# Kernel optimization log

Measured on AMD Instinct MI355X. Metric: run time of the kernel, lower is better.

The kernel has to match this reference:

```python
import jax, jax.numpy as jnp
import numpy as np

N_NODES = 100000
N_EDGES = 1600000
IN_FEATS = 256
H_FEATS = 256
NUM_CLASSES = 64


def setup_inputs() -> dict:
    key = jax.random.key(0)
    ks = jax.random.split(key, 7)
    x = jax.random.normal(ks[0], (N_NODES, IN_FEATS), dtype=jnp.float32)
    src = jax.random.randint(ks[1], (N_EDGES,), 0, N_NODES, dtype=jnp.int64)
    dst = jax.random.randint(ks[2], (N_EDGES,), 0, N_NODES, dtype=jnp.int64)
    W = jax.random.normal(ks[3], (IN_FEATS, H_FEATS), dtype=jnp.float32) / np.sqrt(IN_FEATS)
    b = jax.random.normal(ks[4], (H_FEATS,), dtype=jnp.float32) * 0.01
    W2 = jax.random.normal(ks[5], (H_FEATS, NUM_CLASSES), dtype=jnp.float32) / np.sqrt(H_FEATS)
    b2 = jax.random.normal(ks[6], (NUM_CLASSES,), dtype=jnp.float32) * 0.01
    return {"x": x, "src": src, "dst": dst, "W": W, "b": b, "W2": W2, "b2": b2}


def reference(x, src, dst, W, b, W2, b2):
    N = x.shape[0]
    ones_e = jnp.ones(src.shape[0], dtype=x.dtype)
    # DGL GraphConv norm='both': D_out^{-1/2} on source side, D_in^{-1/2} on dest side
    out_deg = jnp.clip(jax.ops.segment_sum(ones_e, src, num_segments=N), 1.0)
    in_deg = jnp.clip(jax.ops.segment_sum(ones_e, dst, num_segments=N), 1.0)
    h = x * jax.lax.rsqrt(out_deg)[:, None]
    h = h @ W  # [N, h_feats]
    agg = jax.ops.segment_sum(h[src], dst, num_segments=N)  # sparse neighbor aggregation
    agg = agg * jax.lax.rsqrt(in_deg)[:, None] + b
    h = jax.nn.relu(agg)
    pooled = h.mean(axis=0)  # [h_feats]
    logits = pooled @ W2 + b2  # [num_classes]
    return jax.nn.softmax(logits, axis=0)
```

## Files before the change

### kernel.cpp

```cpp
#include <hip/hip_runtime.h>
#include <hip/hip_bf16.h>

#define M_N  100000
#define N_E  1600000
#define FEAT 256
#define NCLS 64
#define SCAN_NB ((M_N + 255) / 256)

typedef __attribute__((ext_vector_type(8))) short bf16x8;
typedef __attribute__((ext_vector_type(4))) float f32x4;

__device__ __forceinline__ ushort f2bf(float f) {
    __hip_bfloat16 h = __float2bfloat16(f);
    return __builtin_bit_cast(ushort, h);
}
__device__ __forceinline__ float bf2f(ushort u) {
    return __uint_as_float(((unsigned)u) << 16);
}
__device__ __forceinline__ void load_lds16(const void* g, void* l) {
    __builtin_amdgcn_global_load_lds(
        (const __attribute__((address_space(1))) void*)g,
        (__attribute__((address_space(3))) void*)l, 16, 0, 0);
}

__global__ void deg_kernel(const int* __restrict__ src, const int* __restrict__ dst,
                           int* __restrict__ cnt_out, int* __restrict__ cnt_in, int nE) {
    int i = blockIdx.x * blockDim.x + threadIdx.x;
    int stride = gridDim.x * blockDim.x;
    for (int e = i; e < nE; e += stride) {
        atomicAdd(&cnt_out[src[e]], 1);
        atomicAdd(&cnt_in[dst[e]], 1);
    }
}

__global__ __launch_bounds__(256) void scanA_kernel(const int* __restrict__ cnt_in,
                                                    int* __restrict__ bsum) {
    __shared__ int sh[256];
    int t = threadIdx.x;
    int i = blockIdx.x * 256 + t;
    sh[t] = (i < M_N) ? cnt_in[i] : 0;
    __syncthreads();
#pragma unroll
    for (int o = 128; o > 0; o >>= 1) {
        if (t < o) sh[t] += sh[t + o];
        __syncthreads();
    }
    if (t == 0) bsum[blockIdx.x] = sh[0];
}

__global__ __launch_bounds__(512) void scanB_kernel(int* __restrict__ bsum) {
    __shared__ int sh[512];
    int t = threadIdx.x;
    int v = (t < SCAN_NB) ? bsum[t] : 0;
    sh[t] = v;
    __syncthreads();
    for (int o = 1; o < 512; o <<= 1) {
        int u = (t >= o) ? sh[t - o] : 0;
        __syncthreads();
        sh[t] += u;
        __syncthreads();
    }
    if (t < SCAN_NB) bsum[t] = sh[t] - v;
}

__global__ __launch_bounds__(256) void scanC_kernel(
    const int* __restrict__ cnt_in, const int* __restrict__ cnt_out,
    const int* __restrict__ bsum, int* __restrict__ row_start,
    int* __restrict__ cursor, float* __restrict__ rs_out) {
    __shared__ int sh[256];
    int t = threadIdx.x;
    int i = blockIdx.x * 256 + t;
    int v = (i < M_N) ? cnt_in[i] : 0;
    sh[t] = v;
    __syncthreads();
    for (int o = 1; o < 256; o <<= 1) {
        int u = (t >= o) ? sh[t - o] : 0;
        __syncthreads();
        sh[t] += u;
        __syncthreads();
    }
    int base = bsum[blockIdx.x];
    int excl = base + sh[t] - v;
    if (i < M_N) {
        row_start[i] = excl;
        cursor[i]    = excl;
        int co = cnt_out[i]; if (co < 1) co = 1;
        rs_out[i] = rsqrtf((float)co);
        if (i == M_N - 1) row_start[M_N] = excl + v;
    }
}

__global__ void bucket_kernel(const int* __restrict__ src, const int* __restrict__ dst,
                              int* __restrict__ cursor, int* __restrict__ csr_src, int nE) {
    int i = blockIdx.x * blockDim.x + threadIdx.x;
    int stride = gridDim.x * blockDim.x;
    for (int e = i; e < nE; e += stride) {
        int pos = atomicAdd(&cursor[dst[e]], 1);
        csr_src[pos] = src[e];
    }
}

__global__ __launch_bounds__(256) void xn_kernel(const float* __restrict__ x,
                                                 const float* __restrict__ rs_out,
                                                 ushort* __restrict__ xn) {
    int i = blockIdx.x * blockDim.x + threadIdx.x;
    int stride = gridDim.x * blockDim.x;
    const int total = M_N * (FEAT / 4);
    for (; i < total; i += stride) {
        int row = i >> 6;
        float r = rs_out[row];
        float4 v = *reinterpret_cast<const float4*>(x + (size_t)i * 4);
        ushort4 o;
        o.x = f2bf(v.x * r); o.y = f2bf(v.y * r);
        o.z = f2bf(v.z * r); o.w = f2bf(v.w * r);
        *reinterpret_cast<ushort4*>(xn + (size_t)i * 4) = o;
    }
}

__global__ void wt_kernel(const float* __restrict__ W, ushort* __restrict__ Wt) {
    int i = blockIdx.x * blockDim.x + threadIdx.x;
    if (i < FEAT * FEAT) {
        int k = i >> 8, n = i & 255;
        Wt[n * FEAT + k] = f2bf(W[i]);
    }
}

__global__ __launch_bounds__(256) void gemm_xw_kernel(
    const ushort* __restrict__ xn, const ushort* __restrict__ Wt,
    ushort* __restrict__ xw) {
    __shared__ ushort As[128 * 32];
    __shared__ ushort Bs[128 * 32];
    const int tid  = threadIdx.x;
    const int lane = tid & 63;
    const int w    = tid >> 6;
    const int wr   = w >> 1, wc = w & 1;
    const int m0   = blockIdx.x * 128;
    const int n0   = blockIdx.y * 128;

    f32x4 acc[4][4];
#pragma unroll
    for (int i = 0; i < 4; ++i)
#pragma unroll
        for (int j = 0; j < 4; ++j) {
            acc[i][j][0] = 0.f; acc[i][j][1] = 0.f;
            acc[i][j][2] = 0.f; acc[i][j][3] = 0.f;
        }

    const int lr = lane >> 2;
    const int lb = (lane & 3) * 16;

    for (int k0 = 0; k0 < FEAT; k0 += 32) {
        __syncthreads();
#pragma unroll
        for (int j = 0; j < 2; ++j) {
            const int seg = (w * 2 + j) * 1024;
            int row = (seg >> 6) + lr;
            int gr = m0 + row; if (gr >= M_N) gr = M_N - 1;
            load_lds16((const char*)xn + (size_t)gr * 512 + k0 * 2 + lb,
                       (char*)As + seg);
            load_lds16((const char*)Wt + (size_t)(n0 + row) * 512 + k0 * 2 + lb,
                       (char*)Bs + seg);
        }
        __syncthreads();
        bf16x8 a[4], b[4];
#pragma unroll
        for (int mi = 0; mi < 4; ++mi) {
            int row = wr * 64 + mi * 16 + (lane & 15);
            a[mi] = *(const bf16x8*)((const char*)As + row * 64 + (lane >> 4) * 16);
        }
#pragma unroll
        for (int ni = 0; ni < 4; ++ni) {
            int n = wc * 64 + ni * 16 + (lane & 15);
            b[ni] = *(const bf16x8*)((const char*)Bs + n * 64 + (lane >> 4) * 16);
        }
#pragma unroll
        for (int mi = 0; mi < 4; ++mi)
#pragma unroll
            for (int ni = 0; ni < 4; ++ni)
                acc[mi][ni] = __builtin_amdgcn_mfma_f32_16x16x32_bf16(
                    a[mi], b[ni], acc[mi][ni], 0, 0, 0);
    }

#pragma unroll
    for (int mi = 0; mi < 4; ++mi) {
        int rbase = m0 + wr * 64 + mi * 16 + (lane >> 4) * 4;
#pragma unroll
        for (int ni = 0; ni < 4; ++ni) {
            int col = n0 + wc * 64 + ni * 16 + (lane & 15);
#pragma unroll
            for (int j = 0; j < 4; ++j) {
                int r = rbase + j;
                if (r < M_N) xw[(size_t)r * FEAT + col] = f2bf(acc[mi][ni][j]);
            }
        }
    }
}

__global__ __launch_bounds__(256) void gather_pool_kernel(
    const ushort* __restrict__ xw, const int* __restrict__ csr_src,
    const int* __restrict__ row_start, const float* __restrict__ bias,
    float* __restrict__ pooled) {
    __shared__ float pool_lds[FEAT];
    int tid = threadIdx.x;
    pool_lds[tid] = 0.0f;
    __syncthreads();
    int lane = tid & 63;
    int wave = tid >> 6;
    int gw = blockIdx.x * 4 + wave;
    int nw = gridDim.x * 4;
    float b0 = bias[lane * 4 + 0], b1 = bias[lane * 4 + 1];
    float b2 = bias[lane * 4 + 2], b3 = bias[lane * 4 + 3];
    float p0 = 0.f, p1 = 0.f, p2 = 0.f, p3 = 0.f;

    for (int d = gw; d < M_N; d += nw) {
        int e0 = row_start[d], e1 = row_start[d + 1];
        float s0 = 0.f, s1 = 0.f, s2 = 0.f, s3 = 0.f;
        int e = e0;
        for (; e + 1 < e1; e += 2) {
            int sa = csr_src[e], sb = csr_src[e + 1];
            ushort4 va = *(const ushort4*)(xw + (size_t)sa * FEAT + lane * 4);
            ushort4 vb = *(const ushort4*)(xw + (size_t)sb * FEAT + lane * 4);
            s0 += bf2f(va.x) + bf2f(vb.x);
            s1 += bf2f(va.y) + bf2f(vb.y);
            s2 += bf2f(va.z) + bf2f(vb.z);
            s3 += bf2f(va.w) + bf2f(vb.w);
        }
        if (e < e1) {
            int sa = csr_src[e];
            ushort4 va = *(const ushort4*)(xw + (size_t)sa * FEAT + lane * 4);
            s0 += bf2f(va.x); s1 += bf2f(va.y); s2 += bf2f(va.z); s3 += bf2f(va.w);
        }
        float ri = rsqrtf(fmaxf((float)(e1 - e0), 1.0f));
        p0 += fmaxf(s0 * ri + b0, 0.f);
        p1 += fmaxf(s1 * ri + b1, 0.f);
        p2 += fmaxf(s2 * ri + b2, 0.f);
        p3 += fmaxf(s3 * ri + b3, 0.f);
    }
    atomicAdd(&pool_lds[lane * 4 + 0], p0);
    atomicAdd(&pool_lds[lane * 4 + 1], p1);
    atomicAdd(&pool_lds[lane * 4 + 2], p2);
    atomicAdd(&pool_lds[lane * 4 + 3], p3);
    __syncthreads();
    atomicAdd(&pooled[tid], pool_lds[tid]);
}

__global__ void final_kernel(const float* __restrict__ pooled, const float* __restrict__ W2,
                             const float* __restrict__ b2, float* __restrict__ out) {
    int c = threadIdx.x;
    const float invN = 1.0f / (float)M_N;
    float acc = 0.0f;
    for (int f = 0; f < FEAT; ++f) acc += pooled[f] * W2[f * NCLS + c];
    acc = acc * invN + b2[c];
    float m = acc;
#pragma unroll
    for (int o = 32; o > 0; o >>= 1) m = fmaxf(m, __shfl_xor(m, o));
    float e = expf(acc - m);
    float s = e;
#pragma unroll
    for (int o = 32; o > 0; o >>= 1) s += __shfl_xor(s, o);
    out[c] = e / s;
}

extern "C" void kernel_launch(void* const* d_in, const int* in_sizes, int n_in,
                              void* d_out, int out_size, void* d_ws, size_t ws_size,
                              hipStream_t stream) {
    const float* x   = (const float*)d_in[0];
    const int*   src = (const int*)d_in[1];
    const int*   dst = (const int*)d_in[2];
    const float* W   = (const float*)d_in[3];
    const float* b   = (const float*)d_in[4];
    const float* W2  = (const float*)d_in[5];
    const float* b2  = (const float*)d_in[6];
    float* out = (float*)d_out;

    char* p = (char*)d_ws;
    ushort* xn       = (ushort*)p;  p += (size_t)M_N * FEAT * 2;
    ushort* xw       = (ushort*)p;  p += (size_t)M_N * FEAT * 2;
    ushort* Wt       = (ushort*)p;  p += (size_t)FEAT * FEAT * 2;
    int*    cnt_out  = (int*)p;     p += (size_t)M_N * 4;
    int*    cnt_in   = (int*)p;     p += (size_t)M_N * 4;
    float*  pooled   = (float*)p;   p += 1024;
    int*    row_start= (int*)p;     p += ((size_t)M_N + 8) * 4;
    int*    cursor   = (int*)p;     p += (size_t)M_N * 4;
    float*  rs_out   = (float*)p;   p += (size_t)M_N * 4;
    int*    bsum     = (int*)p;     p += 2048;
    int*    csr_src  = (int*)p;     p += (size_t)N_E * 4;

    hipMemsetAsync(cnt_out, 0, (size_t)(2 * M_N) * 4 + 1024, stream);

    deg_kernel<<<1024, 256, 0, stream>>>(src, dst, cnt_out, cnt_in, N_E);
    scanA_kernel<<<SCAN_NB, 256, 0, stream>>>(cnt_in, bsum);
    scanB_kernel<<<1, 512, 0, stream>>>(bsum);
    scanC_kernel<<<SCAN_NB, 256, 0, stream>>>(cnt_in, cnt_out, bsum,
                                              row_start, cursor, rs_out);
    bucket_kernel<<<1024, 256, 0, stream>>>(src, dst, cursor, csr_src, N_E);
    xn_kernel<<<2048, 256, 0, stream>>>(x, rs_out, xn);
    wt_kernel<<<(FEAT * FEAT + 255) / 256, 256, 0, stream>>>(W, Wt);
    gemm_xw_kernel<<<dim3((M_N + 127) / 128, 2), 256, 0, stream>>>(xn, Wt, xw);
    gather_pool_kernel<<<2048, 256, 0, stream>>>(xw, csr_src, row_start, b, pooled);
    final_kernel<<<1, 64, 0, stream>>>(pooled, W2, b2, out);
}
```

Baseline: 616.5 us.

## Fuse x normalization and bf16 conversion into GEMM A-tile load; unroll gather by four

Removes the separate xn_kernel and its bf16 intermediate buffer. The GEMM now loads fp32 x rows directly, scales them by the out-degree rsqrt, converts to bf16 in registers and writes them into LDS. This saves a full write and re-read of a 51 MB intermediate, at the cost of reading fp32 x twice (once per N-tile column block) with synchronous register loads instead of async LDS loads. The gather loop is also unrolled to four edges per iteration for more memory-level parallelism.

```diff
diff --git a/kernel.cpp b/kernel.cpp
--- a/kernel.cpp
+++ b/kernel.cpp
@@ -8,6 +8,7 @@
 #define SCAN_NB ((M_N + 255) / 256)
 
 typedef __attribute__((ext_vector_type(8))) short bf16x8;
+typedef __attribute__((ext_vector_type(8))) ushort u16x8;
 typedef __attribute__((ext_vector_type(4))) float f32x4;
 
 __device__ __forceinline__ ushort f2bf(float f) {
@@ -100,23 +101,6 @@
     }
 }
 
-__global__ __launch_bounds__(256) void xn_kernel(const float* __restrict__ x,
-                                                 const float* __restrict__ rs_out,
-                                                 ushort* __restrict__ xn) {
-    int i = blockIdx.x * blockDim.x + threadIdx.x;
-    int stride = gridDim.x * blockDim.x;
-    const int total = M_N * (FEAT / 4);
-    for (; i < total; i += stride) {
-        int row = i >> 6;
-        float r = rs_out[row];
-        float4 v = *reinterpret_cast<const float4*>(x + (size_t)i * 4);
-        ushort4 o;
-        o.x = f2bf(v.x * r); o.y = f2bf(v.y * r);
-        o.z = f2bf(v.z * r); o.w = f2bf(v.w * r);
-        *reinterpret_cast<ushort4*>(xn + (size_t)i * 4) = o;
-    }
-}
-
 __global__ void wt_kernel(const float* __restrict__ W, ushort* __restrict__ Wt) {
     int i = blockIdx.x * blockDim.x + threadIdx.x;
     if (i < FEAT * FEAT) {
@@ -126,8 +110,8 @@
 }
 
 __global__ __launch_bounds__(256) void gemm_xw_kernel(
-    const ushort* __restrict__ xn, const ushort* __restrict__ Wt,
-    ushort* __restrict__ xw) {
+    const float* __restrict__ x, const float* __restrict__ rs_out,
+    const ushort* __restrict__ Wt, ushort* __restrict__ xw) {
     __shared__ ushort As[128 * 32];
     __shared__ ushort Bs[128 * 32];
     const int tid  = threadIdx.x;
@@ -137,6 +121,15 @@
     const int m0   = blockIdx.x * 128;
     const int n0   = blockIdx.y * 128;
 
+    const int ar = tid >> 1;
+    const int ah = tid & 1;
+    int arow = m0 + ar; if (arow >= M_N) arow = M_N - 1;
+    const float rsA = rs_out[arow];
+    const float* xrow = x + (size_t)arow * FEAT + ah * 16;
+
+    const int lr = lane >> 2;
+    const int lb = (lane & 3) * 16;
+
     f32x4 acc[4][4];
 #pragma unroll
     for (int i = 0; i < 4; ++i)
@@ -146,22 +139,32 @@
             acc[i][j][2] = 0.f; acc[i][j][3] = 0.f;
         }
 
-    const int lr = lane >> 2;
-    const int lb = (lane & 3) * 16;
-
     for (int k0 = 0; k0 < FEAT; k0 += 32) {
         __syncthreads();
 #pragma unroll
         for (int j = 0; j < 2; ++j) {
             const int seg = (w * 2 + j) * 1024;
             int row = (seg >> 6) + lr;
-            int gr = m0 + row; if (gr >= M_N) gr = M_N - 1;
-            load_lds16((const char*)xn + (size_t)gr * 512 + k0 * 2 + lb,
-                       (char*)As + seg);
             load_lds16((const char*)Wt + (size_t)(n0 + row) * 512 + k0 * 2 + lb,
                        (char*)Bs + seg);
         }
-        __syncthreads();
+        float4 f0 = *(const float4*)(xrow + k0 + 0);
+        float4 f1 = *(const float4*)(xrow + k0 + 4);
+        float4 f2 = *(const float4*)(xrow + k0 + 8);
+        float4 f3 = *(const float4*)(xrow + k0 + 12);
+        u16x8 lo, hi;
+        lo[0] = f2bf(f0.x * rsA); lo[1] = f2bf(f0.y * rsA);
+        lo[2] = f2bf(f0.z * rsA); lo[3] = f2bf(f0.w * rsA);
+        lo[4] = f2bf(f1.x * rsA); lo[5] = f2bf(f1.y * rsA);
+        lo[6] = f2bf(f1.z * rsA); lo[7] = f2bf(f1.w * rsA);
+        hi[0] = f2bf(f2.x * rsA); hi[1] = f2bf(f2.y * rsA);
+        hi[2] = f2bf(f2.z * rsA); hi[3] = f2bf(f2.w * rsA);
+        hi[4] = f2bf(f3.x * rsA); hi[5] = f2bf(f3.y * rsA);
+        hi[6] = f2bf(f3.z * rsA); hi[7] = f2bf(f3.w * rsA);
+        *(u16x8*)((char*)As + ar * 64 + ah * 32)      = lo;
+        *(u16x8*)((char*)As + ar * 64 + ah * 32 + 16) = hi;
+        __syncthreads();
+
         bf16x8 a[4], b[4];
 #pragma unroll
         for (int mi = 0; mi < 4; ++mi) {
@@ -216,18 +219,21 @@
         int e0 = row_start[d], e1 = row_start[d + 1];
         float s0 = 0.f, s1 = 0.f, s2 = 0.f, s3 = 0.f;
         int e = e0;
-        for (; e + 1 < e1; e += 2) {
-            int sa = csr_src[e], sb = csr_src[e + 1];
-            ushort4 va = *(const ushort4*)(xw + (size_t)sa * FEAT + lane * 4);
-            ushort4 vb = *(const ushort4*)(xw + (size_t)sb * FEAT + lane * 4);
-            s0 += bf2f(va.x) + bf2f(vb.x);
-            s1 += bf2f(va.y) + bf2f(vb.y);
-            s2 += bf2f(va.z) + bf2f(vb.z);
-            s3 += bf2f(va.w) + bf2f(vb.w);
-        }
-        if (e < e1) {
-            int sa = csr_src[e];
-            ushort4 va = *(const ushort4*)(xw + (size_t)sa * FEAT + lane * 4);
+        for (; e + 3 < e1; e += 4) {
+            int ia = csr_src[e], ib = csr_src[e + 1];
+            int ic = csr_src[e + 2], id = csr_src[e + 3];
+            ushort4 va = *(const ushort4*)(xw + (size_t)ia * FEAT + lane * 4);
+            ushort4 vb = *(const ushort4*)(xw + (size_t)ib * FEAT + lane * 4);
+            ushort4 vc = *(const ushort4*)(xw + (size_t)ic * FEAT + lane * 4);
+            ushort4 vd = *(const ushort4*)(xw + (size_t)id * FEAT + lane * 4);
+            s0 += (bf2f(va.x) + bf2f(vb.x)) + (bf2f(vc.x) + bf2f(vd.x));
+            s1 += (bf2f(va.y) + bf2f(vb.y)) + (bf2f(vc.y) + bf2f(vd.y));
+            s2 += (bf2f(va.z) + bf2f(vb.z)) + (bf2f(vc.z) + bf2f(vd.z));
+            s3 += (bf2f(va.w) + bf2f(vb.w)) + (bf2f(vc.w) + bf2f(vd.w));
+        }
+        for (; e < e1; ++e) {
+            int ia = csr_src[e];
+            ushort4 va = *(const ushort4*)(xw + (size_t)ia * FEAT + lane * 4);
             s0 += bf2f(va.x); s1 += bf2f(va.y); s2 += bf2f(va.z); s3 += bf2f(va.w);
         }
         float ri = rsqrtf(fmaxf((float)(e1 - e0), 1.0f));
@@ -274,7 +280,6 @@
     float* out = (float*)d_out;
 
     char* p = (char*)d_ws;
-    ushort* xn       = (ushort*)p;  p += (size_t)M_N * FEAT * 2;
     ushort* xw       = (ushort*)p;  p += (size_t)M_N * FEAT * 2;
     ushort* Wt       = (ushort*)p;  p += (size_t)FEAT * FEAT * 2;
     int*    cnt_out  = (int*)p;     p += (size_t)M_N * 4;
@@ -294,9 +299,8 @@
     scanC_kernel<<<SCAN_NB, 256, 0, stream>>>(cnt_in, cnt_out, bsum,
                                               row_start, cursor, rs_out);
     bucket_kernel<<<1024, 256, 0, stream>>>(src, dst, cursor, csr_src, N_E);
-    xn_kernel<<<2048, 256, 0, stream>>>(x, rs_out, xn);
     wt_kernel<<<(FEAT * FEAT + 255) / 256, 256, 0, stream>>>(W, Wt);
-    gemm_xw_kernel<<<dim3((M_N + 127) / 128, 2), 256, 0, stream>>>(xn, Wt, xw);
+    gemm_xw_kernel<<<dim3((M_N + 127) / 128, 2), 256, 0, stream>>>(x, rs_out, Wt, xw);
     gather_pool_kernel<<<2048, 256, 0, stream>>>(xw, csr_src, row_start, b, pooled);
     final_kernel<<<1, 64, 0, stream>>>(pooled, W2, b2, out);
 }
```

Result: no change. 607.3 us (-1.5%).
